# Kernel tuning notes

Hardware: AMD Instinct MI355X
Metric: run time of the kernel (lower is better)

The kernel has to match this reference:

```python
import jax, jax.numpy as jnp
import numpy as np

TEMPERATURE = 0.5
NEG_FILL = -9e15


def setup_inputs() -> dict:
    key = jax.random.key(0)
    k1, k2 = jax.random.split(key)
    B, D = 4096, 256
    z1 = jax.random.normal(k1, (B, D), dtype=jnp.float32)
    z2 = jax.random.normal(k2, (B, D), dtype=jnp.float32)
    return {"z1": z1, "z2": z2}


def reference(z1, z2):
    B = z1.shape[0]
    z = jnp.concatenate([z1, z2], axis=0)  # [2B, D]
    # cosine similarity: normalize once, then GEMM (same math as broadcast cosine_similarity,
    # torch uses eps=1e-8 clamp on norms)
    norm = jnp.maximum(jnp.linalg.norm(z, axis=1, keepdims=True), 1e-8)
    zn = z / norm
    sim = (zn @ zn.T) / TEMPERATURE  # [2B, 2B]
    # mask self-similarity on the diagonal
    idx = jnp.arange(2 * B)
    sim = sim.at[idx, idx].set(NEG_FILL)
    labels = jnp.concatenate([jnp.arange(B) + B, jnp.arange(B)], axis=0)  # [2B]
    logp = jax.nn.log_softmax(sim, axis=1)
    loss = -jnp.mean(logp[idx, labels])
    return loss
```

## Files before the change

### kernel.cpp

```cpp
#include <hip/hip_runtime.h>

#define N_TOTAL 8192
#define B_HALF  4096
#define D_DIM   256
#define BM      128
#define CSPLIT  8
#define COLS_PER_SPLIT 1024
#define NTILE   8

typedef __attribute__((ext_vector_type(4))) float f32x4;
typedef __attribute__((ext_vector_type(2))) long  long2_t;

#define GLOAD16(src, dst) __builtin_amdgcn_global_load_lds( \
    (const __attribute__((address_space(1))) unsigned int*)(src), \
    (__attribute__((address_space(3))) unsigned int*)(dst), 16, 0, 0)

__global__ __launch_bounds__(256) void nrmpos_kernel(const float* __restrict__ z1,
                                                     const float* __restrict__ z2,
                                                     unsigned char* __restrict__ zn8,
                                                     float* __restrict__ pos) {
    int i    = (blockIdx.x * 256 + threadIdx.x) >> 6;
    int lane = threadIdx.x & 63;
    float4 a = reinterpret_cast<const float4*>(z1 + (size_t)i * D_DIM)[lane];
    float4 b = reinterpret_cast<const float4*>(z2 + (size_t)i * D_DIM)[lane];
    float ssa = a.x * a.x + a.y * a.y + a.z * a.z + a.w * a.w;
    float ssb = b.x * b.x + b.y * b.y + b.z * b.z + b.w * b.w;
    float dab = a.x * b.x + a.y * b.y + a.z * b.z + a.w * b.w;
#pragma unroll
    for (int m = 32; m >= 1; m >>= 1) {
        ssa += __shfl_xor(ssa, m);
        ssb += __shfl_xor(ssb, m);
        dab += __shfl_xor(dab, m);
    }
    float inva = 1.0f / fmaxf(sqrtf(ssa), 1e-8f);
    float invb = 1.0f / fmaxf(sqrtf(ssb), 1e-8f);
    float sa = 1.4142135623730951f * inva;
    float sb = 1.4142135623730951f * invb;
    int pa = __builtin_amdgcn_cvt_pk_fp8_f32(a.x * sa, a.y * sa, 0, false);
    pa     = __builtin_amdgcn_cvt_pk_fp8_f32(a.z * sa, a.w * sa, pa, true);
    int pb = __builtin_amdgcn_cvt_pk_fp8_f32(b.x * sb, b.y * sb, 0, false);
    pb     = __builtin_amdgcn_cvt_pk_fp8_f32(b.z * sb, b.w * sb, pb, true);
    int p = ((lane >> 1) & 3) * 64 + (lane >> 3) * 8 + (lane & 1) * 4;
    *reinterpret_cast<int*>(zn8 + (size_t)i * D_DIM + p)            = pa;
    *reinterpret_cast<int*>(zn8 + (size_t)(i + B_HALF) * D_DIM + p) = pb;
    if (lane == 0) {
        float pp = 2.0f * dab * inva * invb;
        pos[i]          = pp;
        pos[i + B_HALF] = pp;
    }
}

__global__ __launch_bounds__(256, 2) void simexp_kernel(const unsigned char* __restrict__ zn8,
                                                        float* __restrict__ partials) {
    __shared__ __attribute__((aligned(16))) unsigned char lA[BM * D_DIM];
    __shared__ __attribute__((aligned(16))) unsigned char lB[BM * D_DIM];
    __shared__ float red[4][64];

    const int bi = blockIdx.x;
    const int ci = blockIdx.y;
    const int tid  = threadIdx.x;
    const int lane = tid & 63;
    const int wid  = tid >> 6;
    const int wr   = wid >> 1;
    const int wc   = wid & 1;
    const int lrow16 = lane & 15;
    const int kgrp   = lane >> 4;

    const unsigned char* Abase  = zn8 + (size_t)bi * BM * D_DIM;
    const unsigned char* Bbase0 = zn8 + (size_t)ci * COLS_PER_SPLIT * D_DIM;

    int ga[8], soff[8];
#pragma unroll
    for (int u = 0; u < 8; ++u) {
        const int g = tid + u * 256;
        const int r = g >> 4, c = g & 15;
        ga[u]   = g << 4;
        soff[u] = r * D_DIM + ((c ^ (r & 15)) << 4);
    }

    auto stageB = [&](int t) {
        const unsigned char* Bb = Bbase0 + (size_t)t * BM * D_DIM;
#pragma unroll
        for (int u = 0; u < 8; ++u) GLOAD16(Bb + soff[u], lB + ga[u]);
    };

    f32x4 acc[4][4];
    float rowacc[4][4];
#pragma unroll
    for (int mt = 0; mt < 4; ++mt)
#pragma unroll
        for (int nt = 0; nt < 4; ++nt) { acc[mt][nt] = (f32x4)(0.0f); rowacc[mt][nt] = 0.0f; }

#pragma unroll
    for (int u = 0; u < 8; ++u) GLOAD16(Abase + soff[u], lA + ga[u]);
    stageB(0);
    __syncthreads();

    for (int t = 0; t < NTILE; ++t) {
#pragma unroll
        for (int ks2 = 0; ks2 < 4; ++ks2) {
            const int cp = ((kgrp * 4 + ks2) ^ lrow16) << 4;
            long2_t af[4], bf[4];
#pragma unroll
            for (int mt = 0; mt < 4; ++mt)
                af[mt] = *reinterpret_cast<const long2_t*>(
                    lA + (wr * 64 + mt * 16 + lrow16) * D_DIM + cp);
#pragma unroll
            for (int nt = 0; nt < 4; ++nt)
                bf[nt] = *reinterpret_cast<const long2_t*>(
                    lB + (wc * 64 + nt * 16 + lrow16) * D_DIM + cp);
#pragma unroll
            for (int mt = 0; mt < 4; ++mt)
#pragma unroll
                for (int nt = 0; nt < 4; ++nt) {
                    acc[mt][nt] = __builtin_amdgcn_mfma_f32_16x16x32_fp8_fp8(
                        af[mt][0], bf[nt][0], acc[mt][nt], 0, 0, 0);
                    acc[mt][nt] = __builtin_amdgcn_mfma_f32_16x16x32_fp8_fp8(
                        af[mt][1], bf[nt][1], acc[mt][nt], 0, 0, 0);
                }
        }

        __syncthreads();
        if (t + 1 < NTILE) stageB(t + 1);

        const bool dg = (ci * NTILE + t) == bi;
        if (dg) {
#pragma unroll
            for (int mt = 0; mt < 4; ++mt) {
                const int lrowb = wr * 64 + mt * 16 + 4 * kgrp;
#pragma unroll
                for (int r = 0; r < 4; ++r) {
                    const int lrow = lrowb + r;
                    float s = 0.0f;
#pragma unroll
                    for (int nt = 0; nt < 4; ++nt) {
                        const int lcol = wc * 64 + nt * 16 + lrow16;
                        float e = __expf(acc[mt][nt][r] - 2.0f);
                        s += (lrow == lcol) ? 0.0f : e;
                    }
                    rowacc[mt][r] += s;
                }
            }
        } else {
#pragma unroll
            for (int mt = 0; mt < 4; ++mt)
#pragma unroll
                for (int r = 0; r < 4; ++r) {
                    float s = 0.0f;
#pragma unroll
                    for (int nt = 0; nt < 4; ++nt)
                        s += __expf(acc[mt][nt][r] - 2.0f);
                    rowacc[mt][r] += s;
                }
        }
#pragma unroll
        for (int mt = 0; mt < 4; ++mt)
#pragma unroll
            for (int nt = 0; nt < 4; ++nt) acc[mt][nt] = (f32x4)(0.0f);

        if (t + 1 < NTILE) __syncthreads();
    }

#pragma unroll
    for (int mt = 0; mt < 4; ++mt)
#pragma unroll
        for (int r = 0; r < 4; ++r) {
            float v = rowacc[mt][r];
            v += __shfl_xor(v, 1); v += __shfl_xor(v, 2);
            v += __shfl_xor(v, 4); v += __shfl_xor(v, 8);
            if (lrow16 == 0) red[wid][mt * 16 + kgrp * 4 + r] = v;
        }
    __syncthreads();
    if (tid < BM) {
        const int h = tid >> 6, l = tid & 63;
        partials[(size_t)ci * N_TOTAL + bi * BM + tid] = red[h * 2][l] + red[h * 2 + 1][l];
    }
}

__global__ __launch_bounds__(256) void lse_kernel(const float* __restrict__ partials,
                                                  const float* __restrict__ pos,
                                                  float* __restrict__ bsums) {
    int tid = threadIdx.x;
    int row = blockIdx.x * 256 + tid;
    float s = 0.0f;
#pragma unroll
    for (int c = 0; c < CSPLIT; ++c) s += partials[(size_t)c * N_TOTAL + row];
    float v = 2.0f + logf(s) - pos[row];
#pragma unroll
    for (int m = 32; m >= 1; m >>= 1) v += __shfl_xor(v, m);
    __shared__ float wsum[4];
    if ((tid & 63) == 0) wsum[tid >> 6] = v;
    __syncthreads();
    if (tid == 0) bsums[blockIdx.x] = wsum[0] + wsum[1] + wsum[2] + wsum[3];
}

__global__ void final_kernel(const float* __restrict__ bsums, float* __restrict__ out) {
    int tid = threadIdx.x;
    float v = (tid < N_TOTAL / 256) ? bsums[tid] : 0.0f;
#pragma unroll
    for (int m = 32; m >= 1; m >>= 1) v += __shfl_xor(v, m);
    if (tid == 0) out[0] = v * (1.0f / (float)N_TOTAL);
}

extern "C" void kernel_launch(void* const* d_in, const int* in_sizes, int n_in,
                              void* d_out, int out_size, void* d_ws, size_t ws_size,
                              hipStream_t stream) {
    const float* z1 = (const float*)d_in[0];
    const float* z2 = (const float*)d_in[1];
    float* out = (float*)d_out;

    char* ws = (char*)d_ws;
    unsigned char* zn8 = (unsigned char*)ws;
    size_t off = (size_t)N_TOTAL * D_DIM;
    float* pos = (float*)(ws + off);
    off += (size_t)N_TOTAL * sizeof(float);
    float* partials = (float*)(ws + off);
    off += (size_t)CSPLIT * N_TOTAL * sizeof(float);
    float* bsums = (float*)(ws + off);

    nrmpos_kernel<<<B_HALF / 4, 256, 0, stream>>>(z1, z2, zn8, pos);
    simexp_kernel<<<dim3(N_TOTAL / BM, CSPLIT), 256, 0, stream>>>(zn8, partials);
    lse_kernel<<<N_TOTAL / 256, 256, 0, stream>>>(partials, pos, bsums);
    final_kernel<<<1, 64, 0, stream>>>(bsums, out);
}
```

Measured before the change: 40.86 us.

## Double the row tile, double-buffer B in LDS, keep A fragments in registers

```diff
diff --git a/kernel.cpp b/kernel.cpp
--- a/kernel.cpp
+++ b/kernel.cpp
@@ -3,7 +3,7 @@
 #define N_TOTAL 8192
 #define B_HALF  4096
 #define D_DIM   256
-#define BM      128
+#define BM      256
 #define CSPLIT  8
 #define COLS_PER_SPLIT 1024
 #define NTILE   8
@@ -50,11 +50,11 @@
     }
 }
 
-__global__ __launch_bounds__(256, 2) void simexp_kernel(const unsigned char* __restrict__ zn8,
+__global__ __launch_bounds__(512, 2) void simexp_kernel(const unsigned char* __restrict__ zn8,
                                                         float* __restrict__ partials) {
     __shared__ __attribute__((aligned(16))) unsigned char lA[BM * D_DIM];
-    __shared__ __attribute__((aligned(16))) unsigned char lB[BM * D_DIM];
-    __shared__ float red[4][64];
+    __shared__ __attribute__((aligned(16))) unsigned char lB[2][128 * D_DIM];
+    __shared__ float red[8][64];
 
     const int bi = blockIdx.x;
     const int ci = blockIdx.y;
@@ -69,65 +69,84 @@
     const unsigned char* Abase  = zn8 + (size_t)bi * BM * D_DIM;
     const unsigned char* Bbase0 = zn8 + (size_t)ci * COLS_PER_SPLIT * D_DIM;
 
-    int ga[8], soff[8];
+    int soffA[8], soffB[4];
 #pragma unroll
     for (int u = 0; u < 8; ++u) {
-        const int g = tid + u * 256;
+        const int g = tid + u * 512;
         const int r = g >> 4, c = g & 15;
-        ga[u]   = g << 4;
-        soff[u] = r * D_DIM + ((c ^ (r & 15)) << 4);
-    }
-
-    auto stageB = [&](int t) {
-        const unsigned char* Bb = Bbase0 + (size_t)t * BM * D_DIM;
-#pragma unroll
-        for (int u = 0; u < 8; ++u) GLOAD16(Bb + soff[u], lB + ga[u]);
+        soffA[u] = r * D_DIM + ((c ^ (r & 15)) << 4);
+    }
+#pragma unroll
+    for (int u = 0; u < 4; ++u) {
+        const int g = tid + u * 512;
+        const int r = g >> 4, c = g & 15;
+        soffB[u] = r * D_DIM + ((c ^ (r & 15)) << 4);
+    }
+
+    auto stageB = [&](int t, int buf) {
+        const unsigned char* Bb = Bbase0 + (size_t)t * 128 * D_DIM;
+#pragma unroll
+        for (int u = 0; u < 4; ++u)
+            GLOAD16(Bb + soffB[u], lB[buf] + ((tid + u * 512) << 4));
     };
 
-    f32x4 acc[4][4];
+#pragma unroll
+    for (int u = 0; u < 8; ++u)
+        GLOAD16(Abase + soffA[u], lA + ((tid + u * 512) << 4));
+    stageB(0, 0);
+    __syncthreads();
+
+    long2_t aF[4][4];
+#pragma unroll
+    for (int ks2 = 0; ks2 < 4; ++ks2)
+#pragma unroll
+        for (int mt = 0; mt < 4; ++mt)
+            aF[ks2][mt] = *reinterpret_cast<const long2_t*>(
+                lA + (wr * 64 + mt * 16 + lrow16) * D_DIM
+                   + (((kgrp * 4 + ks2) ^ lrow16) << 4));
+
     float rowacc[4][4];
 #pragma unroll
     for (int mt = 0; mt < 4; ++mt)
 #pragma unroll
-        for (int nt = 0; nt < 4; ++nt) { acc[mt][nt] = (f32x4)(0.0f); rowacc[mt][nt] = 0.0f; }
-
-#pragma unroll
-    for (int u = 0; u < 8; ++u) GLOAD16(Abase + soff[u], lA + ga[u]);
-    stageB(0);
-    __syncthreads();
+        for (int r = 0; r < 4; ++r) rowacc[mt][r] = 0.0f;
 
     for (int t = 0; t < NTILE; ++t) {
+        if (t + 1 < NTILE) stageB(t + 1, (t + 1) & 1);
+        const unsigned char* Bl = lB[t & 1];
+
+        f32x4 acc[4][4];
+#pragma unroll
+        for (int mt = 0; mt < 4; ++mt)
+#pragma unroll
+            for (int nt = 0; nt < 4; ++nt) acc[mt][nt] = (f32x4)(0.0f);
+
 #pragma unroll
         for (int ks2 = 0; ks2 < 4; ++ks2) {
-            const int cp = ((kgrp * 4 + ks2) ^ lrow16) << 4;
-            long2_t af[4], bf[4];
-#pragma unroll
-            for (int mt = 0; mt < 4; ++mt)
-                af[mt] = *reinterpret_cast<const long2_t*>(
-                    lA + (wr * 64 + mt * 16 + lrow16) * D_DIM + cp);
+            long2_t bF[4];
 #pragma unroll
             for (int nt = 0; nt < 4; ++nt)
-                bf[nt] = *reinterpret_cast<const long2_t*>(
-                    lB + (wc * 64 + nt * 16 + lrow16) * D_DIM + cp);
+                bF[nt] = *reinterpret_cast<const long2_t*>(
+                    Bl + (wc * 64 + nt * 16 + lrow16) * D_DIM
+                       + (((kgrp * 4 + ks2) ^ lrow16) << 4));
 #pragma unroll
             for (int mt = 0; mt < 4; ++mt)
 #pragma unroll
                 for (int nt = 0; nt < 4; ++nt) {
                     acc[mt][nt] = __builtin_amdgcn_mfma_f32_16x16x32_fp8_fp8(
-                        af[mt][0], bf[nt][0], acc[mt][nt], 0, 0, 0);
+                        aF[ks2][mt][0], bF[nt][0], acc[mt][nt], 0, 0, 0);
                     acc[mt][nt] = __builtin_amdgcn_mfma_f32_16x16x32_fp8_fp8(
-                        af[mt][1], bf[nt][1], acc[mt][nt], 0, 0, 0);
+                        aF[ks2][mt][1], bF[nt][1], acc[mt][nt], 0, 0, 0);
                 }
         }
 
-        __syncthreads();
-        if (t + 1 < NTILE) stageB(t + 1);
-
-        const bool dg = (ci * NTILE + t) == bi;
+        const int cb  = ci * NTILE + t;
+        const bool dg = (cb >> 1) == bi;
+        const int sub = (cb & 1) << 7;
         if (dg) {
 #pragma unroll
             for (int mt = 0; mt < 4; ++mt) {
-                const int lrowb = wr * 64 + mt * 16 + 4 * kgrp;
+                const int lrowb = wr * 64 + mt * 16 + 4 * kgrp - sub;
 #pragma unroll
                 for (int r = 0; r < 4; ++r) {
                     const int lrow = lrowb + r;
@@ -153,12 +172,7 @@
                     rowacc[mt][r] += s;
                 }
         }
-#pragma unroll
-        for (int mt = 0; mt < 4; ++mt)
-#pragma unroll
-            for (int nt = 0; nt < 4; ++nt) acc[mt][nt] = (f32x4)(0.0f);
-
-        if (t + 1 < NTILE) __syncthreads();
+        __syncthreads();
     }
 
 #pragma unroll
@@ -172,8 +186,9 @@
         }
     __syncthreads();
     if (tid < BM) {
-        const int h = tid >> 6, l = tid & 63;
-        partials[(size_t)ci * N_TOTAL + bi * BM + tid] = red[h * 2][l] + red[h * 2 + 1][l];
+        const int wrr = tid >> 6, l = tid & 63;
+        partials[(size_t)ci * N_TOTAL + bi * BM + tid] =
+            red[wrr * 2][l] + red[wrr * 2 + 1][l];
     }
 }
 
@@ -219,7 +234,7 @@
     float* bsums = (float*)(ws + off);
 
     nrmpos_kernel<<<B_HALF / 4, 256, 0, stream>>>(z1, z2, zn8, pos);
-    simexp_kernel<<<dim3(N_TOTAL / BM, CSPLIT), 256, 0, stream>>>(zn8, partials);
+    simexp_kernel<<<dim3(N_TOTAL / BM, CSPLIT), 512, 0, stream>>>(zn8, partials);
     lse_kernel<<<N_TOTAL / 256, 256, 0, stream>>>(partials, pos, bsums);
     final_kernel<<<1, 64, 0, stream>>>(bsums, out);
 }
```

New measurement: 42.44 us. 3.9% more time.

## Double-buffer B tiles, keep A fragments in registers, subtract diagonal analytically

Applied to the files above, without the earlier changes.

```diff
diff --git a/kernel.cpp b/kernel.cpp
--- a/kernel.cpp
+++ b/kernel.cpp
@@ -15,10 +15,18 @@
     (const __attribute__((address_space(1))) unsigned int*)(src), \
     (__attribute__((address_space(3))) unsigned int*)(dst), 16, 0, 0)
 
+__device__ __forceinline__ float fp8_to_f32(unsigned b) {
+    unsigned s = b >> 7, e = (b >> 3) & 15, m = b & 7;
+    float mag = e ? (float)(8 + m) * __int_as_float((int)((e + 117) << 23))
+                  : (float)m * 0.001953125f;
+    return s ? -mag : mag;
+}
+
 __global__ __launch_bounds__(256) void nrmpos_kernel(const float* __restrict__ z1,
                                                      const float* __restrict__ z2,
                                                      unsigned char* __restrict__ zn8,
-                                                     float* __restrict__ pos) {
+                                                     float* __restrict__ pos,
+                                                     float* __restrict__ self) {
     int i    = (blockIdx.x * 256 + threadIdx.x) >> 6;
     int lane = threadIdx.x & 63;
     float4 a = reinterpret_cast<const float4*>(z1 + (size_t)i * D_DIM)[lane];
@@ -40,20 +48,34 @@
     pa     = __builtin_amdgcn_cvt_pk_fp8_f32(a.z * sa, a.w * sa, pa, true);
     int pb = __builtin_amdgcn_cvt_pk_fp8_f32(b.x * sb, b.y * sb, 0, false);
     pb     = __builtin_amdgcn_cvt_pk_fp8_f32(b.z * sb, b.w * sb, pb, true);
+    float sa8 = 0.0f, sb8 = 0.0f;
+#pragma unroll
+    for (int u = 0; u < 4; ++u) {
+        float da = fp8_to_f32((unsigned)(pa >> (8 * u)) & 0xff);
+        float db = fp8_to_f32((unsigned)(pb >> (8 * u)) & 0xff);
+        sa8 += da * da;
+        sb8 += db * db;
+    }
+#pragma unroll
+    for (int m = 32; m >= 1; m >>= 1) {
+        sa8 += __shfl_xor(sa8, m);
+        sb8 += __shfl_xor(sb8, m);
+    }
     int p = ((lane >> 1) & 3) * 64 + (lane >> 3) * 8 + (lane & 1) * 4;
     *reinterpret_cast<int*>(zn8 + (size_t)i * D_DIM + p)            = pa;
     *reinterpret_cast<int*>(zn8 + (size_t)(i + B_HALF) * D_DIM + p) = pb;
     if (lane == 0) {
         float pp = 2.0f * dab * inva * invb;
-        pos[i]          = pp;
-        pos[i + B_HALF] = pp;
+        pos[i]           = pp;
+        pos[i + B_HALF]  = pp;
+        self[i]          = sa8;
+        self[i + B_HALF] = sb8;
     }
 }
 
 __global__ __launch_bounds__(256, 2) void simexp_kernel(const unsigned char* __restrict__ zn8,
                                                         float* __restrict__ partials) {
-    __shared__ __attribute__((aligned(16))) unsigned char lA[BM * D_DIM];
-    __shared__ __attribute__((aligned(16))) unsigned char lB[BM * D_DIM];
+    __shared__ __attribute__((aligned(16))) unsigned char lB[2][BM * D_DIM];
     __shared__ float red[4][64];
 
     const int bi = blockIdx.x;
@@ -69,97 +91,92 @@
     const unsigned char* Abase  = zn8 + (size_t)bi * BM * D_DIM;
     const unsigned char* Bbase0 = zn8 + (size_t)ci * COLS_PER_SPLIT * D_DIM;
 
-    int ga[8], soff[8];
+    int soff[8];
 #pragma unroll
     for (int u = 0; u < 8; ++u) {
         const int g = tid + u * 256;
         const int r = g >> 4, c = g & 15;
-        ga[u]   = g << 4;
         soff[u] = r * D_DIM + ((c ^ (r & 15)) << 4);
     }
-
-    auto stageB = [&](int t) {
+    auto stageB = [&](int t, int buf) {
         const unsigned char* Bb = Bbase0 + (size_t)t * BM * D_DIM;
 #pragma unroll
-        for (int u = 0; u < 8; ++u) GLOAD16(Bb + soff[u], lB + ga[u]);
+        for (int u = 0; u < 8; ++u)
+            GLOAD16(Bb + soff[u], lB[buf] + ((tid + u * 256) << 4));
     };
 
-    f32x4 acc[4][4];
+#pragma unroll
+    for (int u = 0; u < 8; ++u)
+        GLOAD16(Abase + soff[u], lB[1] + ((tid + u * 256) << 4));
+    stageB(0, 0);
+    __syncthreads();
+
+    long2_t aF[4][4];
+#pragma unroll
+    for (int ks2 = 0; ks2 < 4; ++ks2)
+#pragma unroll
+        for (int mt = 0; mt < 4; ++mt)
+            aF[ks2][mt] = *reinterpret_cast<const long2_t*>(
+                lB[1] + (wr * 64 + mt * 16 + lrow16) * D_DIM
+                      + (((kgrp * 4 + ks2) ^ lrow16) << 4));
+    __syncthreads();
+
+    f32x4 accA[4][4], accB[4][4];
     float rowacc[4][4];
 #pragma unroll
     for (int mt = 0; mt < 4; ++mt)
 #pragma unroll
-        for (int nt = 0; nt < 4; ++nt) { acc[mt][nt] = (f32x4)(0.0f); rowacc[mt][nt] = 0.0f; }
-
-#pragma unroll
-    for (int u = 0; u < 8; ++u) GLOAD16(Abase + soff[u], lA + ga[u]);
-    stageB(0);
-    __syncthreads();
-
-    for (int t = 0; t < NTILE; ++t) {
+        for (int nt = 0; nt < 4; ++nt) {
+            accA[mt][nt] = (f32x4)(0.0f);
+            accB[mt][nt] = (f32x4)(0.0f);
+            rowacc[mt][nt] = 0.0f;
+        }
+
+    auto mfma_tile = [&](const unsigned char* Bl, f32x4 (&acc)[4][4]) {
 #pragma unroll
         for (int ks2 = 0; ks2 < 4; ++ks2) {
-            const int cp = ((kgrp * 4 + ks2) ^ lrow16) << 4;
-            long2_t af[4], bf[4];
-#pragma unroll
-            for (int mt = 0; mt < 4; ++mt)
-                af[mt] = *reinterpret_cast<const long2_t*>(
-                    lA + (wr * 64 + mt * 16 + lrow16) * D_DIM + cp);
+            long2_t bF[4];
 #pragma unroll
             for (int nt = 0; nt < 4; ++nt)
-                bf[nt] = *reinterpret_cast<const long2_t*>(
-                    lB + (wc * 64 + nt * 16 + lrow16) * D_DIM + cp);
+                bF[nt] = *reinterpret_cast<const long2_t*>(
+                    Bl + (wc * 64 + nt * 16 + lrow16) * D_DIM
+                       + (((kgrp * 4 + ks2) ^ lrow16) << 4));
 #pragma unroll
             for (int mt = 0; mt < 4; ++mt)
 #pragma unroll
                 for (int nt = 0; nt < 4; ++nt) {
                     acc[mt][nt] = __builtin_amdgcn_mfma_f32_16x16x32_fp8_fp8(
-                        af[mt][0], bf[nt][0], acc[mt][nt], 0, 0, 0);
+                        aF[ks2][mt][0], bF[nt][0], acc[mt][nt], 0, 0, 0);
                     acc[mt][nt] = __builtin_amdgcn_mfma_f32_16x16x32_fp8_fp8(
-                        af[mt][1], bf[nt][1], acc[mt][nt], 0, 0, 0);
+                        aF[ks2][mt][1], bF[nt][1], acc[mt][nt], 0, 0, 0);
                 }
         }
-
-        __syncthreads();
-        if (t + 1 < NTILE) stageB(t + 1);
-
-        const bool dg = (ci * NTILE + t) == bi;
-        if (dg) {
-#pragma unroll
-            for (int mt = 0; mt < 4; ++mt) {
-                const int lrowb = wr * 64 + mt * 16 + 4 * kgrp;
-#pragma unroll
-                for (int r = 0; r < 4; ++r) {
-                    const int lrow = lrowb + r;
-                    float s = 0.0f;
-#pragma unroll
-                    for (int nt = 0; nt < 4; ++nt) {
-                        const int lcol = wc * 64 + nt * 16 + lrow16;
-                        float e = __expf(acc[mt][nt][r] - 2.0f);
-                        s += (lrow == lcol) ? 0.0f : e;
-                    }
-                    rowacc[mt][r] += s;
-                }
+    };
+    auto exp_acc = [&](f32x4 (&acc)[4][4]) {
+#pragma unroll
+        for (int mt = 0; mt < 4; ++mt)
+#pragma unroll
+            for (int r = 0; r < 4; ++r) {
+                float s = 0.0f;
+#pragma unroll
+                for (int nt = 0; nt < 4; ++nt)
+                    s += __expf(acc[mt][nt][r] - 2.0f);
+                rowacc[mt][r] += s;
             }
-        } else {
-#pragma unroll
-            for (int mt = 0; mt < 4; ++mt)
-#pragma unroll
-                for (int r = 0; r < 4; ++r) {
-                    float s = 0.0f;
-#pragma unroll
-                    for (int nt = 0; nt < 4; ++nt)
-                        s += __expf(acc[mt][nt][r] - 2.0f);
-                    rowacc[mt][r] += s;
-                }
-        }
 #pragma unroll
         for (int mt = 0; mt < 4; ++mt)
 #pragma unroll
             for (int nt = 0; nt < 4; ++nt) acc[mt][nt] = (f32x4)(0.0f);
-
-        if (t + 1 < NTILE) __syncthreads();
-    }
+    };
+
+    stageB(1, 1); mfma_tile(lB[0], accA); __syncthreads();
+    for (int tp = 0; tp < 3; ++tp) {
+        const int t = 1 + 2 * tp;
+        stageB(t + 1, 0); mfma_tile(lB[1], accB); exp_acc(accA); __syncthreads();
+        stageB(t + 2, 1); mfma_tile(lB[0], accA); exp_acc(accB); __syncthreads();
+    }
+    mfma_tile(lB[1], accB); exp_acc(accA);
+    exp_acc(accB);
 
 #pragma unroll
     for (int mt = 0; mt < 4; ++mt)
@@ -179,12 +196,14 @@
 
 __global__ __launch_bounds__(256) void lse_kernel(const float* __restrict__ partials,
                                                   const float* __restrict__ pos,
+                                                  const float* __restrict__ self,
                                                   float* __restrict__ bsums) {
     int tid = threadIdx.x;
     int row = blockIdx.x * 256 + tid;
     float s = 0.0f;
 #pragma unroll
     for (int c = 0; c < CSPLIT; ++c) s += partials[(size_t)c * N_TOTAL + row];
+    s -= __expf(self[row] - 2.0f);
     float v = 2.0f + logf(s) - pos[row];
 #pragma unroll
     for (int m = 32; m >= 1; m >>= 1) v += __shfl_xor(v, m);
@@ -214,12 +233,14 @@
     size_t off = (size_t)N_TOTAL * D_DIM;
     float* pos = (float*)(ws + off);
     off += (size_t)N_TOTAL * sizeof(float);
+    float* self = (float*)(ws + off);
+    off += (size_t)N_TOTAL * sizeof(float);
     float* partials = (float*)(ws + off);
     off += (size_t)CSPLIT * N_TOTAL * sizeof(float);
     float* bsums = (float*)(ws + off);
 
-    nrmpos_kernel<<<B_HALF / 4, 256, 0, stream>>>(z1, z2, zn8, pos);
+    nrmpos_kernel<<<B_HALF / 4, 256, 0, stream>>>(z1, z2, zn8, pos, self);
     simexp_kernel<<<dim3(N_TOTAL / BM, CSPLIT), 256, 0, stream>>>(zn8, partials);
-    lse_kernel<<<N_TOTAL / 256, 256, 0, stream>>>(partials, pos, bsums);
+    lse_kernel<<<N_TOTAL / 256, 256, 0, stream>>>(partials, pos, self, bsums);
     final_kernel<<<1, 64, 0, stream>>>(bsums, out);
 }
```

New measurement: 84.55 us. 2.07x slower.
